# Performance work log

Hardware: AMD Instinct MI355X
Metric: run time of the kernel (lower is better)

## Reference

```python
import jax, jax.numpy as jnp
import numpy as np

N = 100_000      # nodes
E = 1_600_000    # edges
EMB = 128        # embedding_size
H = 128          # h_feats
G = 128          # graphs in batch
L = 4            # SAGEConv layers
EPS = 1e-5       # batchnorm eps


def setup_inputs() -> dict:
    key = jax.random.key(0)
    ks = jax.random.split(key, 11)
    in_feat = jax.random.randint(ks[0], (N,), 0, 257)
    src = jax.random.randint(ks[1], (E,), 0, N)
    dst = jax.random.randint(ks[2], (E,), 0, N)
    graph_ids = jnp.sort(jax.random.randint(ks[3], (N,), 0, G))
    s = 1.0 / np.sqrt(H)
    emb = jax.random.normal(ks[4], (257, EMB), jnp.float32) * 0.02
    W_self = jax.random.normal(ks[5], (L, H, H), jnp.float32) * s
    W_neigh = jax.random.normal(ks[6], (L, H, H), jnp.float32) * s
    b = jax.random.normal(ks[7], (L, H), jnp.float32) * 0.01
    gamma = jnp.ones((L, H), jnp.float32)
    beta = jnp.zeros((L, H), jnp.float32)
    prelu_w = jnp.full((L, H), 0.25, jnp.float32)
    return dict(in_feat=in_feat, src=src, dst=dst, graph_ids=graph_ids,
                emb=emb, W_self=W_self, W_neigh=W_neigh, b=b,
                gamma=gamma, beta=beta, prelu_w=prelu_w)


def reference(in_feat, src, dst, graph_ids, emb, W_self, W_neigh, b, gamma, beta, prelu_w):
    n = in_feat.shape[0]
    h = emb[in_feat]  # [N, EMB]
    ones_e = jnp.ones(src.shape[0], h.dtype)
    deg = jnp.clip(jax.ops.segment_sum(ones_e, dst, num_segments=n), 1.0)  # in-degree
    outs = []
    for l in range(L):
        # mean neighbor aggregation (src -> dst)
        agg = jax.ops.segment_sum(h[src], dst, num_segments=n) / deg[:, None]
        rst = h @ W_self[l] + agg @ W_neigh[l] + b[l]
        # PReLU (per-channel), then BatchNorm1d (training-mode batch stats), per DGL SAGEConv order
        rst = jnp.where(rst > 0, rst, prelu_w[l] * rst)
        mu = rst.mean(0)
        var = rst.var(0)
        rst = (rst - mu) * jax.lax.rsqrt(var + EPS) * gamma[l] + beta[l]
        outs.append(rst)
        h = rst
    hcat = jnp.concatenate(outs, axis=1)  # [N, 4H]
    cnt = jnp.clip(jax.ops.segment_sum(jnp.ones(n, hcat.dtype), graph_ids, num_segments=G), 1.0)
    g_vec = jax.ops.segment_sum(hcat, graph_ids, num_segments=G) / cnt[:, None]  # [G, 4H]
    return g_vec
```

## Files before the change

kernel.cpp:

```cpp
#include <hip/hip_runtime.h>
#include <hip/hip_bf16.h>


#define EPS_BN 1e-5f
#define BSH 9
#define BCHUNK 4096
#define PCAP 10240

typedef __attribute__((ext_vector_type(8))) short bf16x8;
typedef __attribute__((ext_vector_type(4))) float f32x4;
typedef __attribute__((address_space(1))) const void gconst_t;
typedef __attribute__((address_space(3))) void ldsv_t;

__global__ __launch_bounds__(256) void k_embed(const int* __restrict__ feat,
                                               const float* __restrict__ emb,
                                               __hip_bfloat162* __restrict__ hb2, int n) {
  int idx = blockIdx.x * 256 + threadIdx.x;
  if (idx < n * 64) {
    int i = idx >> 6, c2 = idx & 63;
    float2 v = ((const float2*)emb)[feat[i] * 64 + c2];
    hb2[idx] = __float22bfloat162_rn(v);
  }
}

__global__ __launch_bounds__(256) void k_wconv(const float* __restrict__ W,
                                               __hip_bfloat16* __restrict__ Wt, int total) {
  int idx = blockIdx.x * 256 + threadIdx.x;
  if (idx < total) {
    int l = idx >> 14, r = idx & 16383, nn = r >> 7, kk = r & 127;
    Wt[idx] = __float2bfloat16(W[(l << 14) + kk * 128 + nn]);
  }
}

__global__ void k_gcount(const int* __restrict__ gid, int* __restrict__ gcnt,
                         int* __restrict__ gstart, int n, int G) {
  int g = blockIdx.x * blockDim.x + threadIdx.x;
  if (g >= G) return;
  int lo0 = 0, hi = n;
  while (lo0 < hi) { int mid = (lo0 + hi) >> 1; if (gid[mid] < g) lo0 = mid + 1; else hi = mid; }
  int lo1 = lo0; hi = n;
  while (lo1 < hi) { int mid = (lo1 + hi) >> 1; if (gid[mid] < g + 1) lo1 = mid + 1; else hi = mid; }
  gstart[g] = lo0;
  gcnt[g] = lo1 - lo0;
}

__global__ __launch_bounds__(256) void k_bhist(const int* __restrict__ dst,
                                               int* __restrict__ bktcnt, int m, int nbkt) {
  __shared__ int h[256];
  int t = threadIdx.x;
  h[t] = 0;
  __syncthreads();
#pragma unroll
  for (int k = 0; k < 4; ++k) {
    int idx = blockIdx.x * BCHUNK + k * 1024 + t * 4;
    if (idx + 4 <= m) {
      int4 d = *(const int4*)&dst[idx];
      atomicAdd(&h[d.x >> BSH], 1);
      atomicAdd(&h[d.y >> BSH], 1);
      atomicAdd(&h[d.z >> BSH], 1);
      atomicAdd(&h[d.w >> BSH], 1);
    } else {
      for (int e = idx; e < m && e < idx + 4; ++e) atomicAdd(&h[dst[e] >> BSH], 1);
    }
  }
  __syncthreads();
  for (int b = t; b < nbkt; b += 256)
    if (h[b]) atomicAdd(&bktcnt[b], h[b]);
}

__global__ void k_bscan(const int* __restrict__ bktcnt, int* __restrict__ bbase,
                        int* __restrict__ bcur, int m, int nbkt) {
  __shared__ int sh[256];
  int t = threadIdx.x;
  int v = (t < nbkt) ? bktcnt[t] : 0;
  sh[t] = v;
  __syncthreads();
  for (int o = 1; o < 256; o <<= 1) {
    int x = (t >= o) ? sh[t - o] : 0;
    __syncthreads();
    sh[t] += x;
    __syncthreads();
  }
  if (t < nbkt) { bbase[t] = sh[t] - v; bcur[t] = sh[t] - v; }
  if (t == 0) bbase[nbkt] = m;
}

__global__ __launch_bounds__(256) void k_bin(const int* __restrict__ src, const int* __restrict__ dst,
                                             int* __restrict__ bcur, uint2* __restrict__ binned,
                                             int m, int nbkt) {
  __shared__ uint2 st[BCHUNK];
  __shared__ int bcnt[256], boff[256], bres[256], wcur[256], ss[256];
  int t = threadIdx.x;
  int e0 = blockIdx.x * BCHUNK;
  int cn = min(BCHUNK, m - e0);
  int sv[16], dv[16];
  for (int b = t; b < 256; b += 256) bcnt[b] = 0;
  __syncthreads();
#pragma unroll
  for (int k = 0; k < 16; ++k) {
    int idx = e0 + k * 256 + t;
    if (idx < e0 + cn) {
      sv[k] = src[idx];
      dv[k] = dst[idx];
      atomicAdd(&bcnt[dv[k] >> BSH], 1);
    } else dv[k] = -1;
  }
  __syncthreads();
  int v = (t < nbkt) ? bcnt[t] : 0;
  ss[t] = v;
  __syncthreads();
  for (int o = 1; o < 256; o <<= 1) {
    int x = (t >= o) ? ss[t - o] : 0;
    __syncthreads();
    ss[t] += x;
    __syncthreads();
  }
  if (t < nbkt) {
    int ex = ss[t] - v;
    boff[t] = ex;
    wcur[t] = ex;
    if (v) bres[t] = atomicAdd(&bcur[t], v);
  }
  __syncthreads();
#pragma unroll
  for (int k = 0; k < 16; ++k) {
    if (dv[k] >= 0) {
      int b = dv[k] >> BSH;
      int p = atomicAdd(&wcur[b], 1);
      st[p] = make_uint2((unsigned)sv[k], (unsigned)dv[k]);
    }
  }
  __syncthreads();
  for (int j = t; j < cn; j += 256) {
    uint2 e = st[j];
    int b = (int)(e.y >> BSH);
    binned[(size_t)bres[b] + (j - boff[b])] = e;
  }
}

__global__ __launch_bounds__(256) void k_cnt(const uint2* __restrict__ binned,
                                             const int* __restrict__ bbase,
                                             int* __restrict__ cnt, int n) {
  __shared__ int h[512];
  int b = blockIdx.x, t = threadIdx.x;
  int base = b << BSH;
  int nn = min(512, n - base);
  h[t] = 0; h[t + 256] = 0;
  __syncthreads();
  int lo = bbase[b], hi = bbase[b + 1];
  for (int j = lo + t; j < hi; j += 256) atomicAdd(&h[(int)binned[j].y - base], 1);
  __syncthreads();
  if (t < nn) cnt[base + t] = h[t];
  if (t + 256 < nn) cnt[base + t + 256] = h[t + 256];
}

__global__ __launch_bounds__(256) void k_scan1(const int* __restrict__ cnt,
                                               int* __restrict__ excl,
                                               int* __restrict__ blk_sums, int n) {
  __shared__ int sh[256];
  int t = threadIdx.x;
  int base = blockIdx.x * 1024 + t * 4;
  int4 v = {0, 0, 0, 0};
  if (base < n) v = *(const int4*)&cnt[base];
  int s = v.x + v.y + v.z + v.w;
  sh[t] = s;
  __syncthreads();
  for (int off = 1; off < 256; off <<= 1) {
    int x = (t >= off) ? sh[t - off] : 0;
    __syncthreads();
    sh[t] += x;
    __syncthreads();
  }
  int ex = sh[t] - s;
  if (t == 255) blk_sums[blockIdx.x] = sh[255];
  if (base < n) {
    excl[base]     = ex;
    excl[base + 1] = ex + v.x;
    excl[base + 2] = ex + v.x + v.y;
    excl[base + 3] = ex + v.x + v.y + v.z;
  }
}

__global__ void k_scan2(int* __restrict__ bs, int nb) {
  __shared__ int sh[128];
  int t = threadIdx.x;
  int v = (t < nb) ? bs[t] : 0;
  sh[t] = v;
  __syncthreads();
  for (int off = 1; off < 128; off <<= 1) {
    int x = (t >= off) ? sh[t - off] : 0;
    __syncthreads();
    sh[t] += x;
    __syncthreads();
  }
  if (t < nb) bs[t] = sh[t] - v;
}

__global__ __launch_bounds__(256) void k_scan3(int* __restrict__ rp, const int* __restrict__ bs,
                                               const int* __restrict__ cnt, int* __restrict__ cursor,
                                               float* __restrict__ deg, int n, int ne) {
  int i = blockIdx.x * 256 + threadIdx.x;
  if (i < n) {
    int r = rp[i] + bs[i >> 10];
    rp[i] = r;
    cursor[i] = r;
    int c = cnt[i];
    deg[i] = (float)(c > 0 ? c : 1);
  }
  if (i == 0) rp[n] = ne;
}

__global__ __launch_bounds__(256) void k_place(const uint2* __restrict__ binned,
                                               const int* __restrict__ bbase,
                                               const int* __restrict__ rp,
                                               int* __restrict__ cursor,
                                               int* __restrict__ csr_src, int n) {
  int b = blockIdx.x, t = threadIdx.x;
  int base = b << BSH;
  int lo = bbase[b], hi = bbase[b + 1], m = hi - lo;
  if (m <= 0) return;
  if (m > PCAP) {
    for (int j = lo + t; j < hi; j += 256) {
      uint2 e = binned[j];
      int p = atomicAdd(&cursor[(int)e.y], 1);
      csr_src[p] = (int)e.x;
    }
    return;
  }
  __shared__ int h[512], loff[512], wc[512], ss[256];
  __shared__ int stage[PCAP];
  h[t] = 0; h[t + 256] = 0;
  __syncthreads();
  for (int j = lo + t; j < hi; j += 256) atomicAdd(&h[(int)binned[j].y - base], 1);
  __syncthreads();
  int a0 = h[2 * t], a1 = h[2 * t + 1];
  int s = a0 + a1;
  ss[t] = s;
  __syncthreads();
  for (int o = 1; o < 256; o <<= 1) {
    int x = (t >= o) ? ss[t - o] : 0;
    __syncthreads();
    ss[t] += x;
    __syncthreads();
  }
  int ex = ss[t] - s;
  loff[2 * t] = ex; loff[2 * t + 1] = ex + a0;
  wc[2 * t] = ex;   wc[2 * t + 1] = ex + a0;
  __syncthreads();
  for (int j = lo + t; j < hi; j += 256) {
    uint2 e = binned[j];
    int p = atomicAdd(&wc[(int)e.y - base], 1);
    stage[p] = (int)e.x;
  }
  __syncthreads();
  int cb = rp[base];
  for (int j = t; j < m; j += 256) csr_src[cb + j] = stage[j];
}

__global__ void k_prep(const float* __restrict__ b0, float* __restrict__ ss0,
                       float* __restrict__ beff0) {
  int t = threadIdx.x;
  ss0[t] = 1.f;
  ss0[128 + t] = 0.f;
  beff0[t] = b0[t];
}

__device__ __forceinline__ void acc8(float* a, uint4 v) {
  float2 f;
  f = __bfloat1622float2(*(const __hip_bfloat162*)&v.x); a[0] += f.x; a[1] += f.y;
  f = __bfloat1622float2(*(const __hip_bfloat162*)&v.y); a[2] += f.x; a[3] += f.y;
  f = __bfloat1622float2(*(const __hip_bfloat162*)&v.z); a[4] += f.x; a[5] += f.y;
  f = __bfloat1622float2(*(const __hip_bfloat162*)&v.w); a[6] += f.x; a[7] += f.y;
}

__global__ __launch_bounds__(256) void k_agg(const uint4* __restrict__ hb4,
                                             const int* __restrict__ rp, const int* __restrict__ csr_src,
                                             const float* __restrict__ deg,
                                             const float* __restrict__ ssl,
                                             const __hip_bfloat16* __restrict__ Wst,
                                             const __hip_bfloat16* __restrict__ Wnt,
                                             __hip_bfloat16* __restrict__ Wst2,
                                             __hip_bfloat16* __restrict__ Wnt2,
                                             uint4* __restrict__ aggb4, int n) {
  int lane = threadIdx.x & 63, wid = threadIdx.x >> 6;
  int g = lane >> 4, lr = lane & 15;
  if (blockIdx.x < 16) {
    int id = blockIdx.x * 256 + threadIdx.x;
    int half = id >> 11;
    int ch = id & 2047;
    const uint4* Wsrc = (const uint4*)(half ? Wnt : Wst);
    uint4* Wdst = (uint4*)(half ? Wnt2 : Wst2);
    uint4 v = Wsrc[ch];
    int k0 = (ch * 8) & 127;
    __hip_bfloat162* pv = (__hip_bfloat162*)&v;
#pragma unroll
    for (int j = 0; j < 4; ++j) {
      float2 f = __bfloat1622float2(pv[j]);
      f.x *= ssl[k0 + 2 * j]; f.y *= ssl[k0 + 2 * j + 1];
      pv[j] = __float22bfloat162_rn(f);
    }
    Wdst[ch] = v;
  }
  for (int i = blockIdx.x * 4 + wid; i < n; i += gridDim.x * 4) {
    int beg = rp[i], end = rp[i + 1];
    float a[8];
#pragma unroll
    for (int c = 0; c < 8; ++c) a[c] = 0.f;
    int e = beg;
    for (; e + 8 <= end; e += 8) {
      int s0 = csr_src[e + g];
      int s1 = csr_src[e + 4 + g];
      uint4 v0 = hb4[(size_t)s0 * 16 + lr];
      uint4 v1 = hb4[(size_t)s1 * 16 + lr];
      acc8(a, v0);
      acc8(a, v1);
    }
    for (; e + g < end; e += 4) {
      int s = csr_src[e + g];
      uint4 v = hb4[(size_t)s * 16 + lr];
      acc8(a, v);
    }
#pragma unroll
    for (int c = 0; c < 8; ++c) {
      a[c] += __shfl_xor(a[c], 16, 64);
      a[c] += __shfl_xor(a[c], 32, 64);
    }
    if (g == 0) {
      float v[8];
      if (beg == end) {
#pragma unroll
        for (int c = 0; c < 8; ++c) {
          float sc = ssl[lr * 8 + c], sh = ssl[128 + lr * 8 + c];
          v[c] = (sc != 0.f) ? (-sh / sc) : 0.f;
        }
      } else {
        float invd = 1.0f / deg[i];
#pragma unroll
        for (int c = 0; c < 8; ++c) v[c] = a[c] * invd;
      }
      __hip_bfloat162 p0 = __float22bfloat162_rn(make_float2(v[0], v[1]));
      __hip_bfloat162 p1 = __float22bfloat162_rn(make_float2(v[2], v[3]));
      __hip_bfloat162 p2 = __float22bfloat162_rn(make_float2(v[4], v[5]));
      __hip_bfloat162 p3 = __float22bfloat162_rn(make_float2(v[6], v[7]));
      uint4 o;
      o.x = *(unsigned int*)&p0; o.y = *(unsigned int*)&p1;
      o.z = *(unsigned int*)&p2; o.w = *(unsigned int*)&p3;
      aggb4[(size_t)i * 16 + lr] = o;
    }
  }
}

__global__ __launch_bounds__(256) void k_gemm_fused(
    const __hip_bfloat16* __restrict__ hb, const __hip_bfloat16* __restrict__ aggb,
    const __hip_bfloat16* __restrict__ Wst2, const __hip_bfloat16* __restrict__ Wnt2,
    const float* __restrict__ beff, const float* __restrict__ pw,
    __hip_bfloat16* __restrict__ hbn, float* __restrict__ partial, int n) {
  __shared__ short Ah[128 * 128];
  __shared__ short Aa[128 * 128];
  __shared__ float ls[128], lq[128];
  int t = threadIdx.x;
  int row0 = blockIdx.x * 128;
  if (t < 128) { ls[t] = 0.f; lq[t] = 0.f; }
  int w = t >> 6, lane = t & 63;

#pragma unroll
  for (int rd = 0; rd < 8; ++rd) {
    int Gq = rd * 256 + w * 64 + lane;
    int r = Gq >> 4;
    int gq = (Gq & 15) ^ (r & 7);
    int grow = row0 + r;
    grow = grow < n ? grow : n - 1;
    const __hip_bfloat16* gs = hb   + (size_t)grow * 128 + gq * 8;
    const __hip_bfloat16* ga = aggb + (size_t)grow * 128 + gq * 8;
    __builtin_amdgcn_global_load_lds((gconst_t*)gs,
        (ldsv_t*)&Ah[(rd * 256 + w * 64) * 8], 16, 0, 0);
    __builtin_amdgcn_global_load_lds((gconst_t*)ga,
        (ldsv_t*)&Aa[(rd * 256 + w * 64) * 8], 16, 0, 0);
  }
  asm volatile("s_waitcnt vmcnt(0)" ::: "memory");
  __syncthreads();

  int lr16 = lane & 15, hi = lane >> 4;
  f32x4 acc[2][8];
#pragma unroll
  for (int fm = 0; fm < 2; ++fm)
#pragma unroll
    for (int fn = 0; fn < 8; ++fn) acc[fm][fn] = (f32x4){0.f, 0.f, 0.f, 0.f};

  const short* As[2] = {Ah, Aa};
  const __hip_bfloat16* Bt[2] = {Wst2, Wnt2};
#pragma unroll
  for (int s = 0; s < 2; ++s) {
    const short* A = As[s];
    const __hip_bfloat16* B = Bt[s];
#pragma unroll
    for (int ks = 0; ks < 4; ++ks) {
      bf16x8 af[2], bfr[8];
#pragma unroll
      for (int fm = 0; fm < 2; ++fm) {
        int rl = w * 32 + fm * 16 + lr16;
        int gq = (ks * 4 + hi) ^ (lr16 & 7);
        af[fm] = *(const bf16x8*)&A[rl * 128 + gq * 8];
      }
#pragma unroll
      for (int fn = 0; fn < 8; ++fn)
        bfr[fn] = *(const bf16x8*)(B + (size_t)(fn * 16 + lr16) * 128 + ks * 32 + hi * 8);
#pragma unroll
      for (int fm = 0; fm < 2; ++fm)
#pragma unroll
        for (int fn = 0; fn < 8; ++fn)
          acc[fm][fn] = __builtin_amdgcn_mfma_f32_16x16x32_bf16(af[fm], bfr[fn], acc[fm][fn], 0, 0, 0);
    }
  }

  int rb = hi * 4;
  float sacc[8], qacc[8];
#pragma unroll
  for (int fn = 0; fn < 8; ++fn) { sacc[fn] = 0.f; qacc[fn] = 0.f; }
#pragma unroll
  for (int fm = 0; fm < 2; ++fm) {
    int rbase = row0 + w * 32 + fm * 16 + rb;
#pragma unroll
    for (int fn = 0; fn < 8; ++fn) {
      int col = fn * 16 + lr16;
      float bb = beff[col], pp = pw[col];
#pragma unroll
      for (int r = 0; r < 4; ++r) {
        int grow = rbase + r;
        if (grow < n) {
          float v = acc[fm][fn][r] + bb;
          v = v > 0.f ? v : pp * v;
          hbn[(size_t)grow * 128 + col] = __float2bfloat16(v);
          sacc[fn] += v; qacc[fn] += v * v;
        }
      }
    }
  }
#pragma unroll
  for (int fn = 0; fn < 8; ++fn) {
    int col = fn * 16 + lr16;
    atomicAdd(&ls[col], sacc[fn]);
    atomicAdd(&lq[col], qacc[fn]);
  }
  __syncthreads();
  if (t < 128) {
    float* pp2 = partial + (size_t)(blockIdx.x >> 3) * 256;
    atomicAdd(&pp2[t], ls[t]);
    atomicAdd(&pp2[128 + t], lq[t]);
  }
}

__global__ __launch_bounds__(1024) void k_bnfin(const float* __restrict__ partial, int nb,
                                                const float* __restrict__ gamma,
                                                const float* __restrict__ beta,
                                                float* __restrict__ ss,
                                                const float* __restrict__ bias_next,
                                                const float* __restrict__ Ws_next,
                                                const float* __restrict__ Wn_next,
                                                float* __restrict__ beff_next,
                                                int has_next, int n) {
  __shared__ float red[4][256];
  __shared__ float shv[128];
  __shared__ float bred[8][128];
  int t = threadIdx.x, c = t & 255, part = t >> 8;
  float s = 0.f;
  for (int b = part; b < nb; b += 4) s += partial[(size_t)b * 256 + c];
  red[part][c] = s;
  __syncthreads();
  if (part == 0) red[0][c] = red[0][c] + red[1][c] + red[2][c] + red[3][c];
  __syncthreads();
  if (t < 128) {
    float inv_n = 1.0f / (float)n;
    float mu = red[0][t] * inv_n;
    float var = red[0][128 + t] * inv_n - mu * mu;
    float sc = rsqrtf(var + EPS_BN) * gamma[t];
    float sh = beta[t] - mu * sc;
    ss[t] = sc;
    ss[128 + t] = sh;
    shv[t] = sh;
  }
  __syncthreads();
  if (has_next) {
    int cc = t & 127, kg = t >> 7;
    float acc = 0.f;
#pragma unroll
    for (int k = kg * 16; k < kg * 16 + 16; ++k)
      acc += shv[k] * (Ws_next[k * 128 + cc] + Wn_next[k * 128 + cc]);
    bred[kg][cc] = acc;
    __syncthreads();
    if (t < 128) {
      float r = bias_next[t];
#pragma unroll
      for (int kg2 = 0; kg2 < 8; ++kg2) r += bred[kg2][t];
      beff_next[t] = r;
    }
  }
}

__global__ __launch_bounds__(256) void k_pool(const uint4* __restrict__ hb4,
                                              const int* __restrict__ gstart,
                                              const int* __restrict__ gcnt,
                                              float* __restrict__ out, int l) {
  __shared__ float red[4][128];
  int g = blockIdx.x >> 3, c = blockIdx.x & 7;
  int len = gcnt[g];
  int i0 = gstart[g] + ((len * c) >> 3);
  int i1 = gstart[g] + ((len * (c + 1)) >> 3);
  if (i0 >= i1) return;
  int t = threadIdx.x, w = t >> 6, lane = t & 63;
  int gi = lane >> 4, lr = lane & 15;
  float a[8];
#pragma unroll
  for (int cc = 0; cc < 8; ++cc) a[cc] = 0.f;
#pragma unroll 2
  for (int r = i0 + w * 4 + gi; r < i1; r += 16) {
    uint4 v = hb4[(size_t)r * 16 + lr];
    acc8(a, v);
  }
#pragma unroll
  for (int cc = 0; cc < 8; ++cc) {
    a[cc] += __shfl_xor(a[cc], 16, 64);
    a[cc] += __shfl_xor(a[cc], 32, 64);
  }
  if (gi == 0) {
#pragma unroll
    for (int cc = 0; cc < 8; ++cc) red[w][lr * 8 + cc] = a[cc];
  }
  __syncthreads();
  if (t < 128)
    atomicAdd(&out[(size_t)g * 512 + l * 128 + t],
              red[0][t] + red[1][t] + red[2][t] + red[3][t]);
}

__global__ __launch_bounds__(256) void k_div(float* __restrict__ out, const int* __restrict__ gcnt,
                                             const float* __restrict__ ssbuf, int m) {
  int i = blockIdx.x * 256 + threadIdx.x;
  if (i < m) {
    int g = i >> 9;
    int lc = i & 511;
    int l = lc >> 7, c = lc & 127;
    const float* ss = ssbuf + (l + 1) * 256;
    int cn = gcnt[g];
    out[i] = (cn > 0) ? (out[i] / (float)cn) * ss[c] + ss[128 + c] : 0.f;
  }
}

extern "C" void kernel_launch(void* const* d_in, const int* in_sizes, int n_in,
                              void* d_out, int out_size, void* d_ws, size_t ws_size,
                              hipStream_t stream) {
  const int*   in_feat = (const int*)d_in[0];
  const int*   src     = (const int*)d_in[1];
  const int*   dst     = (const int*)d_in[2];
  const int*   gid     = (const int*)d_in[3];
  const float* emb     = (const float*)d_in[4];
  const float* Wself   = (const float*)d_in[5];
  const float* Wneigh  = (const float*)d_in[6];
  const float* bvec    = (const float*)d_in[7];
  const float* gamma   = (const float*)d_in[8];
  const float* beta    = (const float*)d_in[9];
  const float* prelu   = (const float*)d_in[10];
  const int N = in_sizes[0];
  const int E = in_sizes[1];
  const int G = out_size / 512;
  float* out = (float*)d_out;
  const int NB = (N + 127) / 128;
  const int NP = (NB + 7) / 8;
  const int NBKT = (N + 511) >> BSH;

  char* p = (char*)d_ws;
  size_t off = 0;
  auto take = [&](size_t bytes) { void* r = p + off; off += (bytes + 255) & ~(size_t)255; return r; };
  __hip_bfloat16* hb0   = (__hip_bfloat16*)take((size_t)N * 128 * 2);
  __hip_bfloat16* hb1   = (__hip_bfloat16*)take((size_t)N * 128 * 2);
  __hip_bfloat16* aggb  = (__hip_bfloat16*)take((size_t)N * 128 * 2);
  __hip_bfloat16* Wst   = (__hip_bfloat16*)take((size_t)4 * 128 * 128 * 2);
  __hip_bfloat16* Wnt   = (__hip_bfloat16*)take((size_t)4 * 128 * 128 * 2);
  __hip_bfloat16* Wst2  = (__hip_bfloat16*)take((size_t)128 * 128 * 2);
  __hip_bfloat16* Wnt2  = (__hip_bfloat16*)take((size_t)128 * 128 * 2);
  float* partial        = (float*)take((size_t)NP * 256 * 4);
  float* ssbuf          = (float*)take((size_t)5 * 256 * 4);
  float* beff           = (float*)take((size_t)4 * 128 * 4);
  uint2* binned  = (uint2*)take((size_t)E * 8);
  int*   csr_src = (int*)take((size_t)E * 4);
  int*   cnt     = (int*)take((size_t)N * 4);
  int*   rp      = (int*)take((size_t)(N + 1) * 4);
  int*   cursor  = (int*)take((size_t)N * 4);
  float* deg     = (float*)take((size_t)N * 4);
  int*   bs      = (int*)take(512);
  int*   gcnt    = (int*)take((size_t)G * 4);
  int*   gstart  = (int*)take((size_t)G * 4);
  int*   bktcnt  = (int*)take((size_t)NBKT * 4);
  int*   bbase   = (int*)take((size_t)(NBKT + 1) * 4);
  int*   bcur    = (int*)take((size_t)NBKT * 4);
  if (off > ws_size) return;

  hipMemsetAsync(bktcnt, 0, (size_t)NBKT * 4, stream);
  hipMemsetAsync(d_out, 0, (size_t)out_size * 4, stream);

  k_embed<<<(N * 64 + 255) / 256, 256, 0, stream>>>(in_feat, emb, (__hip_bfloat162*)hb0, N);
  k_wconv<<<(4 * 128 * 128 + 255) / 256, 256, 0, stream>>>(Wself, Wst, 4 * 128 * 128);
  k_wconv<<<(4 * 128 * 128 + 255) / 256, 256, 0, stream>>>(Wneigh, Wnt, 4 * 128 * 128);
  k_gcount<<<1, 128, 0, stream>>>(gid, gcnt, gstart, N, G);

  int nbb = (E + BCHUNK - 1) / BCHUNK;
  k_bhist<<<nbb, 256, 0, stream>>>(dst, bktcnt, E, NBKT);
  k_bscan<<<1, 256, 0, stream>>>(bktcnt, bbase, bcur, E, NBKT);
  k_bin<<<nbb, 256, 0, stream>>>(src, dst, bcur, binned, E, NBKT);
  k_cnt<<<NBKT, 256, 0, stream>>>(binned, bbase, cnt, N);
  int nsb = (N + 1023) / 1024;
  k_scan1<<<nsb, 256, 0, stream>>>(cnt, rp, bs, N);
  k_scan2<<<1, 128, 0, stream>>>(bs, nsb);
  k_scan3<<<(N + 255) / 256, 256, 0, stream>>>(rp, bs, cnt, cursor, deg, N, E);
  k_place<<<NBKT, 256, 0, stream>>>(binned, bbase, rp, cursor, csr_src, N);
  k_prep<<<1, 128, 0, stream>>>(bvec, ssbuf, beff);

  __hip_bfloat16* bufs[2] = {hb0, hb1};
  for (int l = 0; l < 4; ++l) {
    __hip_bfloat16* hin  = bufs[l & 1];
    __hip_bfloat16* hout = bufs[(l + 1) & 1];
    k_agg<<<2048, 256, 0, stream>>>((const uint4*)hin, rp, csr_src, deg,
                                    ssbuf + l * 256,
                                    Wst + l * 16384, Wnt + l * 16384, Wst2, Wnt2,
                                    (uint4*)aggb, N);
    hipMemsetAsync(partial, 0, (size_t)NP * 256 * 4, stream);
    k_gemm_fused<<<NB, 256, 0, stream>>>(hin, aggb, Wst2, Wnt2,
                                         beff + l * 128, prelu + l * 128,
                                         hout, partial, N);
    k_bnfin<<<1, 1024, 0, stream>>>(partial, NP, gamma + l * 128, beta + l * 128,
                                    ssbuf + (l + 1) * 256,
                                    bvec + ((l + 1) & 3) * 128,
                                    Wself + ((l + 1) & 3) * 16384,
                                    Wneigh + ((l + 1) & 3) * 16384,
                                    beff + ((l + 1) & 3) * 128,
                                    (l < 3) ? 1 : 0, N);
    k_pool<<<G * 8, 256, 0, stream>>>((const uint4*)hout, gstart, gcnt, out, l);
  }
  k_div<<<(out_size + 255) / 256, 256, 0, stream>>>(out, gcnt, ssbuf, out_size);
}
```

Measured before the change: 684.6 us.

## Transform before aggregating: GEMM node features first, then gather projected neighbours

Uses linearity of mean aggregation to compute h@W_self and h@W_neigh per node first, then gathers and averages the projected neighbour rows in a fused kernel that also adds bias, applies PReLU and accumulates BatchNorm statistics. The separate aggregation buffer and the dual-input fused GEMM are replaced by a single-input two-output GEMM plus gather-finish. Weight scaling for the next layer's BN folding and zeroing of the partial-stats buffer move into k_bnfin, which removes the per-layer memset. It writes two projected N×128 buffers instead of one aggregate, adding write traffic and an extra bf16 rounding of the neighbour projections before summation.

```diff
diff --git a/kernel.cpp b/kernel.cpp
--- a/kernel.cpp
+++ b/kernel.cpp
@@ -6,6 +6,8 @@
 #define BSH 9
 #define BCHUNK 4096
 #define PCAP 10240
+#define AGG_BLOCKS 2048
+#define NPSLOT 64
 
 typedef __attribute__((ext_vector_type(8))) short bf16x8;
 typedef __attribute__((ext_vector_type(4))) float f32x4;
@@ -257,12 +259,90 @@
   for (int j = t; j < m; j += 256) csr_src[cb + j] = stage[j];
 }
 
-__global__ void k_prep(const float* __restrict__ b0, float* __restrict__ ss0,
-                       float* __restrict__ beff0) {
+__global__ __launch_bounds__(256) void k_prep(const float* __restrict__ b0,
+                                              float* __restrict__ ss0,
+                                              float* __restrict__ beffS0,
+                                              float* __restrict__ cN0,
+                                              const uint4* __restrict__ Wst0,
+                                              const uint4* __restrict__ Wnt0,
+                                              uint4* __restrict__ Ws2,
+                                              uint4* __restrict__ Wn2) {
+  int id = blockIdx.x * 256 + threadIdx.x;
+  if (id < 128) {
+    ss0[id] = 1.f; ss0[128 + id] = 0.f;
+    beffS0[id] = b0[id]; cN0[id] = 0.f;
+  }
+  int half = id >> 11, ch = id & 2047;
+  if (half) Wn2[ch] = Wnt0[ch]; else Ws2[ch] = Wst0[ch];
+}
+
+__global__ __launch_bounds__(256) void k_gemm2(
+    const __hip_bfloat16* __restrict__ hb,
+    const __hip_bfloat16* __restrict__ Wst2, const __hip_bfloat16* __restrict__ Wnt2,
+    __hip_bfloat16* __restrict__ Ys, __hip_bfloat16* __restrict__ Yn, int n) {
+  __shared__ short Ah[128 * 128];
   int t = threadIdx.x;
-  ss0[t] = 1.f;
-  ss0[128 + t] = 0.f;
-  beff0[t] = b0[t];
+  int row0 = blockIdx.x * 128;
+  int w = t >> 6, lane = t & 63;
+
+#pragma unroll
+  for (int rd = 0; rd < 8; ++rd) {
+    int Gq = rd * 256 + w * 64 + lane;
+    int r = Gq >> 4;
+    int gq = (Gq & 15) ^ (r & 7);
+    int grow = row0 + r;
+    grow = grow < n ? grow : n - 1;
+    const __hip_bfloat16* gs = hb + (size_t)grow * 128 + gq * 8;
+    __builtin_amdgcn_global_load_lds((gconst_t*)gs,
+        (ldsv_t*)&Ah[(rd * 256 + w * 64) * 8], 16, 0, 0);
+  }
+  asm volatile("s_waitcnt vmcnt(0)" ::: "memory");
+  __syncthreads();
+
+  int lr16 = lane & 15, hi = lane >> 4;
+  const __hip_bfloat16* Bt[2] = {Wst2, Wnt2};
+  __hip_bfloat16* Ot[2] = {Ys, Yn};
+#pragma unroll
+  for (int s = 0; s < 2; ++s) {
+    const __hip_bfloat16* B = Bt[s];
+    f32x4 acc[2][8];
+#pragma unroll
+    for (int fm = 0; fm < 2; ++fm)
+#pragma unroll
+      for (int fn = 0; fn < 8; ++fn) acc[fm][fn] = (f32x4){0.f, 0.f, 0.f, 0.f};
+#pragma unroll
+    for (int ks = 0; ks < 4; ++ks) {
+      bf16x8 af[2], bfr[8];
+#pragma unroll
+      for (int fm = 0; fm < 2; ++fm) {
+        int rl = w * 32 + fm * 16 + lr16;
+        int gq = (ks * 4 + hi) ^ (lr16 & 7);
+        af[fm] = *(const bf16x8*)&Ah[rl * 128 + gq * 8];
+      }
+#pragma unroll
+      for (int fn = 0; fn < 8; ++fn)
+        bfr[fn] = *(const bf16x8*)(B + (size_t)(fn * 16 + lr16) * 128 + ks * 32 + hi * 8);
+#pragma unroll
+      for (int fm = 0; fm < 2; ++fm)
+#pragma unroll
+        for (int fn = 0; fn < 8; ++fn)
+          acc[fm][fn] = __builtin_amdgcn_mfma_f32_16x16x32_bf16(af[fm], bfr[fn], acc[fm][fn], 0, 0, 0);
+    }
+    __hip_bfloat16* O = Ot[s];
+#pragma unroll
+    for (int fm = 0; fm < 2; ++fm) {
+      int rbase = row0 + w * 32 + fm * 16 + hi * 4;
+#pragma unroll
+      for (int fn = 0; fn < 8; ++fn) {
+        int col = fn * 16 + lr16;
+#pragma unroll
+        for (int r = 0; r < 4; ++r) {
+          int grow = rbase + r;
+          if (grow < n) O[(size_t)grow * 128 + col] = __float2bfloat16(acc[fm][fn][r]);
+        }
+      }
+    }
+  }
 }
 
 __device__ __forceinline__ void acc8(float* a, uint4 v) {
@@ -273,34 +353,29 @@
   f = __bfloat1622float2(*(const __hip_bfloat162*)&v.w); a[6] += f.x; a[7] += f.y;
 }
 
-__global__ __launch_bounds__(256) void k_agg(const uint4* __restrict__ hb4,
-                                             const int* __restrict__ rp, const int* __restrict__ csr_src,
-                                             const float* __restrict__ deg,
-                                             const float* __restrict__ ssl,
-                                             const __hip_bfloat16* __restrict__ Wst,
-                                             const __hip_bfloat16* __restrict__ Wnt,
-                                             __hip_bfloat16* __restrict__ Wst2,
-                                             __hip_bfloat16* __restrict__ Wnt2,
-                                             uint4* __restrict__ aggb4, int n) {
-  int lane = threadIdx.x & 63, wid = threadIdx.x >> 6;
+__global__ __launch_bounds__(256) void k_aggfin(
+    const uint4* __restrict__ yn4, const int* __restrict__ rp,
+    const int* __restrict__ csr_src, const float* __restrict__ deg,
+    const uint4* __restrict__ ys4,
+    const float* __restrict__ beffS, const float* __restrict__ cN,
+    const float* __restrict__ pw,
+    uint4* __restrict__ hbn4, float* __restrict__ partial, int n) {
+  __shared__ float ls[128], lq[128];
+  int t = threadIdx.x;
+  int lane = t & 63, wid = t >> 6;
   int g = lane >> 4, lr = lane & 15;
-  if (blockIdx.x < 16) {
-    int id = blockIdx.x * 256 + threadIdx.x;
-    int half = id >> 11;
-    int ch = id & 2047;
-    const uint4* Wsrc = (const uint4*)(half ? Wnt : Wst);
-    uint4* Wdst = (uint4*)(half ? Wnt2 : Wst2);
-    uint4 v = Wsrc[ch];
-    int k0 = (ch * 8) & 127;
-    __hip_bfloat162* pv = (__hip_bfloat162*)&v;
-#pragma unroll
-    for (int j = 0; j < 4; ++j) {
-      float2 f = __bfloat1622float2(pv[j]);
-      f.x *= ssl[k0 + 2 * j]; f.y *= ssl[k0 + 2 * j + 1];
-      pv[j] = __float22bfloat162_rn(f);
-    }
-    Wdst[ch] = v;
-  }
+  if (t < 128) { ls[t] = 0.f; lq[t] = 0.f; }
+  __syncthreads();
+
+  float bS[8], cn8[8], pw8[8], sacc[8], qacc[8];
+#pragma unroll
+  for (int c = 0; c < 8; ++c) {
+    bS[c] = beffS[lr * 8 + c];
+    cn8[c] = cN[lr * 8 + c];
+    pw8[c] = pw[lr * 8 + c];
+    sacc[c] = 0.f; qacc[c] = 0.f;
+  }
+
   for (int i = blockIdx.x * 4 + wid; i < n; i += gridDim.x * 4) {
     int beg = rp[i], end = rp[i + 1];
     float a[8];
@@ -310,14 +385,14 @@
     for (; e + 8 <= end; e += 8) {
       int s0 = csr_src[e + g];
       int s1 = csr_src[e + 4 + g];
-      uint4 v0 = hb4[(size_t)s0 * 16 + lr];
-      uint4 v1 = hb4[(size_t)s1 * 16 + lr];
+      uint4 v0 = yn4[(size_t)s0 * 16 + lr];
+      uint4 v1 = yn4[(size_t)s1 * 16 + lr];
       acc8(a, v0);
       acc8(a, v1);
     }
     for (; e + g < end; e += 4) {
       int s = csr_src[e + g];
-      uint4 v = hb4[(size_t)s * 16 + lr];
+      uint4 v = yn4[(size_t)s * 16 + lr];
       acc8(a, v);
     }
 #pragma unroll
@@ -326,17 +401,23 @@
       a[c] += __shfl_xor(a[c], 32, 64);
     }
     if (g == 0) {
+      uint4 ysv = ys4[(size_t)i * 16 + lr];
+      float y[8];
+      float2 f;
+      f = __bfloat1622float2(*(const __hip_bfloat162*)&ysv.x); y[0] = f.x; y[1] = f.y;
+      f = __bfloat1622float2(*(const __hip_bfloat162*)&ysv.y); y[2] = f.x; y[3] = f.y;
+      f = __bfloat1622float2(*(const __hip_bfloat162*)&ysv.z); y[4] = f.x; y[5] = f.y;
+      f = __bfloat1622float2(*(const __hip_bfloat162*)&ysv.w); y[6] = f.x; y[7] = f.y;
+      float invd = 1.0f / deg[i];
+      bool has = (beg < end);
       float v[8];
-      if (beg == end) {
-#pragma unroll
-        for (int c = 0; c < 8; ++c) {
-          float sc = ssl[lr * 8 + c], sh = ssl[128 + lr * 8 + c];
-          v[c] = (sc != 0.f) ? (-sh / sc) : 0.f;
-        }
-      } else {
-        float invd = 1.0f / deg[i];
-#pragma unroll
-        for (int c = 0; c < 8; ++c) v[c] = a[c] * invd;
+#pragma unroll
+      for (int c = 0; c < 8; ++c) {
+        float x = y[c] + bS[c];
+        if (has) x += a[c] * invd + cn8[c];
+        x = x > 0.f ? x : pw8[c] * x;
+        sacc[c] += x; qacc[c] += x * x;
+        v[c] = x;
       }
       __hip_bfloat162 p0 = __float22bfloat162_rn(make_float2(v[0], v[1]));
       __hip_bfloat162 p1 = __float22bfloat162_rn(make_float2(v[2], v[3]));
@@ -345,123 +426,41 @@
       uint4 o;
       o.x = *(unsigned int*)&p0; o.y = *(unsigned int*)&p1;
       o.z = *(unsigned int*)&p2; o.w = *(unsigned int*)&p3;
-      aggb4[(size_t)i * 16 + lr] = o;
-    }
-  }
-}
-
-__global__ __launch_bounds__(256) void k_gemm_fused(
-    const __hip_bfloat16* __restrict__ hb, const __hip_bfloat16* __restrict__ aggb,
-    const __hip_bfloat16* __restrict__ Wst2, const __hip_bfloat16* __restrict__ Wnt2,
-    const float* __restrict__ beff, const float* __restrict__ pw,
-    __hip_bfloat16* __restrict__ hbn, float* __restrict__ partial, int n) {
-  __shared__ short Ah[128 * 128];
-  __shared__ short Aa[128 * 128];
-  __shared__ float ls[128], lq[128];
-  int t = threadIdx.x;
-  int row0 = blockIdx.x * 128;
-  if (t < 128) { ls[t] = 0.f; lq[t] = 0.f; }
-  int w = t >> 6, lane = t & 63;
-
-#pragma unroll
-  for (int rd = 0; rd < 8; ++rd) {
-    int Gq = rd * 256 + w * 64 + lane;
-    int r = Gq >> 4;
-    int gq = (Gq & 15) ^ (r & 7);
-    int grow = row0 + r;
-    grow = grow < n ? grow : n - 1;
-    const __hip_bfloat16* gs = hb   + (size_t)grow * 128 + gq * 8;
-    const __hip_bfloat16* ga = aggb + (size_t)grow * 128 + gq * 8;
-    __builtin_amdgcn_global_load_lds((gconst_t*)gs,
-        (ldsv_t*)&Ah[(rd * 256 + w * 64) * 8], 16, 0, 0);
-    __builtin_amdgcn_global_load_lds((gconst_t*)ga,
-        (ldsv_t*)&Aa[(rd * 256 + w * 64) * 8], 16, 0, 0);
-  }
-  asm volatile("s_waitcnt vmcnt(0)" ::: "memory");
-  __syncthreads();
-
-  int lr16 = lane & 15, hi = lane >> 4;
-  f32x4 acc[2][8];
-#pragma unroll
-  for (int fm = 0; fm < 2; ++fm)
-#pragma unroll
-    for (int fn = 0; fn < 8; ++fn) acc[fm][fn] = (f32x4){0.f, 0.f, 0.f, 0.f};
-
-  const short* As[2] = {Ah, Aa};
-  const __hip_bfloat16* Bt[2] = {Wst2, Wnt2};
-#pragma unroll
-  for (int s = 0; s < 2; ++s) {
-    const short* A = As[s];
-    const __hip_bfloat16* B = Bt[s];
-#pragma unroll
-    for (int ks = 0; ks < 4; ++ks) {
-      bf16x8 af[2], bfr[8];
-#pragma unroll
-      for (int fm = 0; fm < 2; ++fm) {
-        int rl = w * 32 + fm * 16 + lr16;
-        int gq = (ks * 4 + hi) ^ (lr16 & 7);
-        af[fm] = *(const bf16x8*)&A[rl * 128 + gq * 8];
-      }
-#pragma unroll
-      for (int fn = 0; fn < 8; ++fn)
-        bfr[fn] = *(const bf16x8*)(B + (size_t)(fn * 16 + lr16) * 128 + ks * 32 + hi * 8);
-#pragma unroll
-      for (int fm = 0; fm < 2; ++fm)
-#pragma unroll
-        for (int fn = 0; fn < 8; ++fn)
-          acc[fm][fn] = __builtin_amdgcn_mfma_f32_16x16x32_bf16(af[fm], bfr[fn], acc[fm][fn], 0, 0, 0);
-    }
-  }
-
-  int rb = hi * 4;
-  float sacc[8], qacc[8];
-#pragma unroll
-  for (int fn = 0; fn < 8; ++fn) { sacc[fn] = 0.f; qacc[fn] = 0.f; }
-#pragma unroll
-  for (int fm = 0; fm < 2; ++fm) {
-    int rbase = row0 + w * 32 + fm * 16 + rb;
-#pragma unroll
-    for (int fn = 0; fn < 8; ++fn) {
-      int col = fn * 16 + lr16;
-      float bb = beff[col], pp = pw[col];
-#pragma unroll
-      for (int r = 0; r < 4; ++r) {
-        int grow = rbase + r;
-        if (grow < n) {
-          float v = acc[fm][fn][r] + bb;
-          v = v > 0.f ? v : pp * v;
-          hbn[(size_t)grow * 128 + col] = __float2bfloat16(v);
-          sacc[fn] += v; qacc[fn] += v * v;
-        }
-      }
-    }
-  }
-#pragma unroll
-  for (int fn = 0; fn < 8; ++fn) {
-    int col = fn * 16 + lr16;
-    atomicAdd(&ls[col], sacc[fn]);
-    atomicAdd(&lq[col], qacc[fn]);
+      hbn4[(size_t)i * 16 + lr] = o;
+    }
+  }
+  if (g == 0) {
+#pragma unroll
+    for (int c = 0; c < 8; ++c) {
+      atomicAdd(&ls[lr * 8 + c], sacc[c]);
+      atomicAdd(&lq[lr * 8 + c], qacc[c]);
+    }
   }
   __syncthreads();
   if (t < 128) {
-    float* pp2 = partial + (size_t)(blockIdx.x >> 3) * 256;
-    atomicAdd(&pp2[t], ls[t]);
-    atomicAdd(&pp2[128 + t], lq[t]);
-  }
-}
-
-__global__ __launch_bounds__(1024) void k_bnfin(const float* __restrict__ partial, int nb,
+    float* pp = partial + (size_t)(blockIdx.x >> 5) * 256;
+    atomicAdd(&pp[t], ls[t]);
+    atomicAdd(&pp[128 + t], lq[t]);
+  }
+}
+
+__global__ __launch_bounds__(1024) void k_bnfin(float* __restrict__ partial, int nb,
                                                 const float* __restrict__ gamma,
                                                 const float* __restrict__ beta,
                                                 float* __restrict__ ss,
                                                 const float* __restrict__ bias_next,
-                                                const float* __restrict__ Ws_next,
-                                                const float* __restrict__ Wn_next,
-                                                float* __restrict__ beff_next,
+                                                const float* __restrict__ Wsf_next,
+                                                const float* __restrict__ Wnf_next,
+                                                const __hip_bfloat16* __restrict__ Wst_next,
+                                                const __hip_bfloat16* __restrict__ Wnt_next,
+                                                __hip_bfloat16* __restrict__ Ws2,
+                                                __hip_bfloat16* __restrict__ Wn2,
+                                                float* __restrict__ beffS_next,
+                                                float* __restrict__ cN_next,
                                                 int has_next, int n) {
   __shared__ float red[4][256];
-  __shared__ float shv[128];
-  __shared__ float bred[8][128];
+  __shared__ float shv[128], scv[128];
+  __shared__ float bredS[8][128], bredN[8][128];
   int t = threadIdx.x, c = t & 255, part = t >> 8;
   float s = 0.f;
   for (int b = part; b < nb; b += 4) s += partial[(size_t)b * 256 + c];
@@ -478,23 +477,35 @@
     ss[t] = sc;
     ss[128 + t] = sh;
     shv[t] = sh;
+    scv[t] = sc;
   }
   __syncthreads();
   if (has_next) {
     int cc = t & 127, kg = t >> 7;
-    float acc = 0.f;
-#pragma unroll
-    for (int k = kg * 16; k < kg * 16 + 16; ++k)
-      acc += shv[k] * (Ws_next[k * 128 + cc] + Wn_next[k * 128 + cc]);
-    bred[kg][cc] = acc;
+    float aS = 0.f, aN = 0.f;
+#pragma unroll
+    for (int k = kg * 16; k < kg * 16 + 16; ++k) {
+      float sh = shv[k];
+      aS += sh * Wsf_next[k * 128 + cc];
+      aN += sh * Wnf_next[k * 128 + cc];
+    }
+    bredS[kg][cc] = aS;
+    bredN[kg][cc] = aN;
     __syncthreads();
     if (t < 128) {
-      float r = bias_next[t];
-#pragma unroll
-      for (int kg2 = 0; kg2 < 8; ++kg2) r += bred[kg2][t];
-      beff_next[t] = r;
-    }
-  }
+      float rS = bias_next[t], rN = 0.f;
+#pragma unroll
+      for (int kg2 = 0; kg2 < 8; ++kg2) { rS += bredS[kg2][t]; rN += bredN[kg2][t]; }
+      beffS_next[t] = rS;
+      cN_next[t] = rN;
+    }
+    for (int i = t; i < 16384; i += 1024) {
+      float scf = scv[i & 127];
+      Ws2[i] = __float2bfloat16(__bfloat162float(Wst_next[i]) * scf);
+      Wn2[i] = __float2bfloat16(__bfloat162float(Wnt_next[i]) * scf);
+    }
+  }
+  for (int i = t; i < nb * 256; i += 1024) partial[i] = 0.f;
 }
 
 __global__ __launch_bounds__(256) void k_pool(const uint4* __restrict__ hb4,
@@ -564,7 +575,6 @@
   const int G = out_size / 512;
   float* out = (float*)d_out;
   const int NB = (N + 127) / 128;
-  const int NP = (NB + 7) / 8;
   const int NBKT = (N + 511) >> BSH;
 
   char* p = (char*)d_ws;
@@ -572,14 +582,16 @@
   auto take = [&](size_t bytes) { void* r = p + off; off += (bytes + 255) & ~(size_t)255; return r; };
   __hip_bfloat16* hb0   = (__hip_bfloat16*)take((size_t)N * 128 * 2);
   __hip_bfloat16* hb1   = (__hip_bfloat16*)take((size_t)N * 128 * 2);
-  __hip_bfloat16* aggb  = (__hip_bfloat16*)take((size_t)N * 128 * 2);
+  __hip_bfloat16* Ysb   = (__hip_bfloat16*)take((size_t)N * 128 * 2);
+  __hip_bfloat16* Ynb   = (__hip_bfloat16*)take((size_t)N * 128 * 2);
   __hip_bfloat16* Wst   = (__hip_bfloat16*)take((size_t)4 * 128 * 128 * 2);
   __hip_bfloat16* Wnt   = (__hip_bfloat16*)take((size_t)4 * 128 * 128 * 2);
   __hip_bfloat16* Wst2  = (__hip_bfloat16*)take((size_t)128 * 128 * 2);
   __hip_bfloat16* Wnt2  = (__hip_bfloat16*)take((size_t)128 * 128 * 2);
-  float* partial        = (float*)take((size_t)NP * 256 * 4);
+  float* partial        = (float*)take((size_t)NPSLOT * 256 * 4);
   float* ssbuf          = (float*)take((size_t)5 * 256 * 4);
-  float* beff           = (float*)take((size_t)4 * 128 * 4);
+  float* beffS          = (float*)take((size_t)4 * 128 * 4);
+  float* cNb            = (float*)take((size_t)4 * 128 * 4);
   uint2* binned  = (uint2*)take((size_t)E * 8);
   int*   csr_src = (int*)take((size_t)E * 4);
   int*   cnt     = (int*)take((size_t)N * 4);
@@ -595,6 +607,7 @@
   if (off > ws_size) return;
 
   hipMemsetAsync(bktcnt, 0, (size_t)NBKT * 4, stream);
+  hipMemsetAsync(partial, 0, (size_t)NPSLOT * 256 * 4, stream);
   hipMemsetAsync(d_out, 0, (size_t)out_size * 4, stream);
 
   k_embed<<<(N * 64 + 255) / 256, 256, 0, stream>>>(in_feat, emb, (__hip_bfloat162*)hb0, N);
@@ -612,26 +625,30 @@
   k_scan2<<<1, 128, 0, stream>>>(bs, nsb);
   k_scan3<<<(N + 255) / 256, 256, 0, stream>>>(rp, bs, cnt, cursor, deg, N, E);
   k_place<<<NBKT, 256, 0, stream>>>(binned, bbase, rp, cursor, csr_src, N);
-  k_prep<<<1, 128, 0, stream>>>(bvec, ssbuf, beff);
+  k_prep<<<16, 256, 0, stream>>>(bvec, ssbuf, beffS, cNb,
+                                 (const uint4*)Wst, (const uint4*)Wnt,
+                                 (uint4*)Wst2, (uint4*)Wnt2);
 
   __hip_bfloat16* bufs[2] = {hb0, hb1};
   for (int l = 0; l < 4; ++l) {
     __hip_bfloat16* hin  = bufs[l & 1];
     __hip_bfloat16* hout = bufs[(l + 1) & 1];
-    k_agg<<<2048, 256, 0, stream>>>((const uint4*)hin, rp, csr_src, deg,
-                                    ssbuf + l * 256,
-                                    Wst + l * 16384, Wnt + l * 16384, Wst2, Wnt2,
-                                    (uint4*)aggb, N);
-    hipMemsetAsync(partial, 0, (size_t)NP * 256 * 4, stream);
-    k_gemm_fused<<<NB, 256, 0, stream>>>(hin, aggb, Wst2, Wnt2,
-                                         beff + l * 128, prelu + l * 128,
-                                         hout, partial, N);
-    k_bnfin<<<1, 1024, 0, stream>>>(partial, NP, gamma + l * 128, beta + l * 128,
+    k_gemm2<<<NB, 256, 0, stream>>>(hin, Wst2, Wnt2, Ysb, Ynb, N);
+    k_aggfin<<<AGG_BLOCKS, 256, 0, stream>>>((const uint4*)Ynb, rp, csr_src, deg,
+                                             (const uint4*)Ysb,
+                                             beffS + l * 128, cNb + l * 128,
+                                             prelu + l * 128,
+                                             (uint4*)hout, partial, N);
+    k_bnfin<<<1, 1024, 0, stream>>>(partial, NPSLOT, gamma + l * 128, beta + l * 128,
                                     ssbuf + (l + 1) * 256,
                                     bvec + ((l + 1) & 3) * 128,
                                     Wself + ((l + 1) & 3) * 16384,
                                     Wneigh + ((l + 1) & 3) * 16384,
-                                    beff + ((l + 1) & 3) * 128,
+                                    Wst + ((l + 1) & 3) * 16384,
+                                    Wnt + ((l + 1) & 3) * 16384,
+                                    Wst2, Wnt2,
+                                    beffS + ((l + 1) & 3) * 128,
+                                    cNb + ((l + 1) & 3) * 128,
                                     (l < 3) ? 1 : 0, N);
     k_pool<<<G * 8, 256, 0, stream>>>((const uint4*)hout, gstart, gcnt, out, l);
   }
```

Result: no change. 698.1 us (+2.0%).
